# Kernel tuning notes

Hardware: AMD Instinct MI355X
Metric: run time of the kernel (lower is better)

The kernel has to match this reference:

```python
import jax, jax.numpy as jnp
import numpy as np
from jax import lax

EPS = 1e-5
DW_THRESH = 4.0
PW_THRESH = 1e-3


def setup_inputs() -> dict:
    key = jax.random.key(0)
    ks = jax.random.split(key, 13)
    B, C, O, H, W = 32, 256, 256, 56, 56
    inp = {
        "x": jax.random.normal(ks[0], (B, C, H, W), jnp.float32),
        "dw_w": jax.random.normal(ks[1], (C, 1, 3, 3), jnp.float32) * 0.2,
        "dw_b": jax.random.normal(ks[2], (C,), jnp.float32) * 0.1,
        "bn1_gamma": 0.5 + jax.random.uniform(ks[3], (C,), jnp.float32) * 1.5,
        "bn1_beta": jax.random.normal(ks[4], (C,), jnp.float32) * 0.5,
        "bn1_mean": jax.random.normal(ks[5], (C,), jnp.float32) * 0.1,
        "bn1_var": 0.5 + jax.random.uniform(ks[6], (C,), jnp.float32),
        "pw_w": jax.random.normal(ks[7], (O, C, 1, 1), jnp.float32) * 0.06,
        "pw_b": jax.random.normal(ks[8], (O,), jnp.float32) * 0.1,
        "bn2_gamma": 0.5 + jax.random.uniform(ks[9], (O,), jnp.float32) * 1.5,
        "bn2_beta": jax.random.normal(ks[10], (O,), jnp.float32) * 0.5,
        "bn2_mean": jax.random.normal(ks[11], (O,), jnp.float32) * 0.1,
        "bn2_var": 0.5 + jax.random.uniform(ks[12], (O,), jnp.float32),
    }
    return inp


def _bn(x, gamma, beta, mean, var):
    # inference-mode BatchNorm2d over channel axis 1
    inv = gamma * lax.rsqrt(var + EPS)
    return x * inv[None, :, None, None] + (beta - mean * inv)[None, :, None, None]


def _cut(x, thresh):
    # per-(batch, channel) max-abs pruning: max(max(x), -min(x)) == max(|x|)
    max_abs = jnp.max(jnp.abs(x), axis=(2, 3))  # [B, C]
    return jnp.where((max_abs < thresh)[:, :, None, None], 0.0, x)


def reference(x, dw_w, dw_b, bn1_gamma, bn1_beta, bn1_mean, bn1_var,
              pw_w, pw_b, bn2_gamma, bn2_beta, bn2_mean, bn2_var):
    C = x.shape[1]
    # depthwise 3x3 conv, padding=1, groups=C
    y = lax.conv_general_dilated(
        x, dw_w, window_strides=(1, 1), padding=[(1, 1), (1, 1)],
        feature_group_count=C,
        dimension_numbers=("NCHW", "OIHW", "NCHW"),
    ) + dw_b[None, :, None, None]
    y = jax.nn.relu(_bn(y, bn1_gamma, bn1_beta, bn1_mean, bn1_var))
    y = _cut(y, DW_THRESH)
    # pointwise 1x1 conv as channel contraction
    z = jnp.einsum("bihw,oi->bohw", y, pw_w[:, :, 0, 0]) + pw_b[None, :, None, None]
    z = jax.nn.relu(_bn(z, bn2_gamma, bn2_beta, bn2_mean, bn2_var))
    z = _cut(z, PW_THRESH)
    return z
```

## Files before the change

### kernel.cpp

```cpp
#include <hip/hip_runtime.h>
#include <hip/hip_bf16.h>
#include <stdint.h>

#define BATCH 32
#define CIN   256
#define COUT  256
#define HW    3136
#define NPAD  3200

#define AS1 __attribute__((address_space(1)))
#define AS3 __attribute__((address_space(3)))

typedef short bf16x8 __attribute__((ext_vector_type(8)));
typedef float f32x4  __attribute__((ext_vector_type(4)));

__device__ __forceinline__ unsigned short f2bf(float f) {
    unsigned u = __float_as_uint(f);
    u += 0x7fffu + ((u >> 16) & 1u);
    return (unsigned short)(u >> 16);
}

__global__ __launch_bounds__(256) void prep_kernel(
        const float* __restrict__ pw_w, const float* __restrict__ pw_b,
        const float* __restrict__ g2, const float* __restrict__ be2,
        const float* __restrict__ mu2, const float* __restrict__ va2,
        unsigned short* __restrict__ Wp, float* __restrict__ b2,
        unsigned* __restrict__ pwmax) {
    int o = blockIdx.x;
    int t = threadIdx.x;
    float inv2 = g2[o] * rsqrtf(va2[o] + 1e-5f);
    Wp[o * CIN + t] = f2bf(pw_w[o * CIN + t] * inv2);
    if (t == 0) b2[o] = pw_b[o] * inv2 + be2[o] - mu2[o] * inv2;
    int idx = blockIdx.x * 256 + t;
    if (idx < BATCH * COUT) pwmax[idx] = 0u;
}

__global__ __launch_bounds__(256) void dw_kernel(
        const float* __restrict__ x, const float* __restrict__ dww,
        const float* __restrict__ dwb,
        const float* __restrict__ g1, const float* __restrict__ be1,
        const float* __restrict__ mu1, const float* __restrict__ va1,
        unsigned short* __restrict__ y) {
    __shared__ float xs[4 * 3136];
    int tid  = threadIdx.x;
    int lane = tid & 63, wid = tid >> 6;
    int plane = blockIdx.x * 4 + wid;
    int c = plane & 255;

    const float* xp = x + (size_t)plane * HW;
    float* xw = xs + wid * 3136;

#pragma unroll
    for (int i = 0; i < 12; ++i)
        __builtin_amdgcn_global_load_lds(
            (const AS1 void*)(xp + i * 256 + lane * 4),
            (AS3 void*)(xw + i * 256), 16, 0, 0);
    __builtin_amdgcn_global_load_lds(
        (const AS1 void*)(xp + 3072 + lane),
        (AS3 void*)(xw + 3072), 4, 0, 0);

    float w00 = dww[c*9+0], w01 = dww[c*9+1], w02 = dww[c*9+2];
    float w10 = dww[c*9+3], w11 = dww[c*9+4], w12 = dww[c*9+5];
    float w20 = dww[c*9+6], w21 = dww[c*9+7], w22 = dww[c*9+8];
    float inv = g1[c] * rsqrtf(va1[c] + 1e-5f);
    float b0  = dwb[c] * inv + (be1[c] - mu1[c] * inv);

    int  col    = lane < 56 ? lane : 55;
    bool active = lane < 56;
    if (lane == 0)  { w00 = 0.f; w10 = 0.f; w20 = 0.f; }
    if (lane >= 55) { w02 = 0.f; w12 = 0.f; w22 = 0.f; }
    int il = (lane == 0) ? 0 : col - 1;
    int ir = (col == 55) ? 55 : col + 1;

    asm volatile("s_waitcnt vmcnt(0)" ::: "memory");
    __builtin_amdgcn_sched_barrier(0);

    const float* xb = xw;
    unsigned short* yp = y + (size_t)plane * NPAD + col;

    float A = 0.f;
    float Bv = 0.f;
    float lmax = 0.f;
#pragma unroll
    for (int q = 0; q < 56; q += 2) {
        float l0 = xb[q*56 + il],      c0 = xb[q*56 + col],      r0 = xb[q*56 + ir];
        float l1 = xb[(q+1)*56 + il],  c1 = xb[(q+1)*56 + col],  r1 = xb[(q+1)*56 + ir];
        if (q > 0) {
            float o0 = fmaf(l0, w20, fmaf(c0, w21, fmaf(r0, w22, A)));
            float v = fmaxf(fmaf(o0, inv, b0), 0.f);
            if (active) { lmax = fmaxf(lmax, v); yp[(q-1)*56] = f2bf(v); }
        }
        {
            float o1 = fmaf(l0, w10, fmaf(c0, w11, fmaf(r0, w12,
                       fmaf(l1, w20, fmaf(c1, w21, fmaf(r1, w22, Bv))))));
            float v = fmaxf(fmaf(o1, inv, b0), 0.f);
            if (active) { lmax = fmaxf(lmax, v); yp[q*56] = f2bf(v); }
        }
        float top0 = fmaf(l0, w00, fmaf(c0, w01, r0 * w02));
        A  = fmaf(l1, w10, fmaf(c1, w11, fmaf(r1, w12, top0)));
        Bv = fmaf(l1, w00, fmaf(c1, w01, r1 * w02));
    }
    {
        float v = fmaxf(fmaf(A, inv, b0), 0.f);
        if (active) { lmax = fmaxf(lmax, v); yp[55*56] = f2bf(v); }
    }
    for (int off = 32; off >= 1; off >>= 1)
        lmax = fmaxf(lmax, __shfl_xor(lmax, off, 64));
    if (lane < 8) *(uint4*)(y + (size_t)plane * NPAD + HW + lane * 8)
        = make_uint4(0, 0, 0, 0);
    if (lmax < 4.0f) {
        asm volatile("s_waitcnt vmcnt(0)" ::: "memory");
        unsigned short* yp0 = y + (size_t)plane * NPAD;
#pragma unroll
        for (int it = 0; it < 7; ++it) {
            int idx = it * 64 + lane;
            if (idx < 392) *(uint4*)(yp0 + idx * 8) = make_uint4(0, 0, 0, 0);
        }
    }
}

__global__ __launch_bounds__(256, 3) void pw_kernel(
        const unsigned short* __restrict__ y, const unsigned short* __restrict__ Wp,
        const float* __restrict__ b2, float* __restrict__ z,
        unsigned* __restrict__ pwmax) {
    __shared__ __align__(16) char lds[32768 + 16384];
    char* Al = lds;

    int bid0 = blockIdx.x;
    int bid  = (bid0 & 7) * 400 + (bid0 >> 3);
    int nt   = bid % 25;
    int rest = bid / 25;
    int ot   = rest & 3;
    int b    = rest >> 2;
    int o0 = ot * 64, n0 = nt * 128;

    int tid = threadIdx.x, lane = tid & 63, wid = tid >> 6;
    char* Bw = lds + 32768 + wid * 4096;
    int wn = wid * 32;
    int l15 = lane & 15, l4 = lane >> 4;

    const unsigned short* yb = y + (size_t)b * CIN * NPAD;

#pragma unroll
    for (int i = 0; i < 8; ++i) {
        int s = i * 256 + tid;
        int m = s >> 5, cch = s & 31, dch = cch ^ (m & 7);
        __builtin_amdgcn_global_load_lds(
            (const AS1 void*)(Wp + (size_t)(o0 + m) * CIN + dch * 8),
            (AS3 void*)(Al + i * 4096 + wid * 1024), 16, 0, 0);
    }

    int l3 = lane & 7, q3 = lane >> 3;
    const unsigned short* bbase = yb + n0 + wn + l3 * 4 + (size_t)(q3 * 4) * NPAD;

    uint2 praw[2][4];
#define LOADB(kk) { _Pragma("unroll") for (int i = 0; i < 2; ++i)             \
                    _Pragma("unroll") for (int r = 0; r < 4; ++r)             \
                      praw[i][r] = *(const uint2*)(bbase +                    \
                          ((size_t)(kk) * 64 + i * 32 + r) * NPAD); }

#define PACKB() { _Pragma("unroll") for (int i = 0; i < 2; ++i) {             \
        int q = i * 8 + q3;                                                   \
        uint2 r0 = praw[i][0], r1 = praw[i][1], r2 = praw[i][2], r3 = praw[i][3]; \
        _Pragma("unroll") for (int i2 = 0; i2 < 4; ++i2) {                    \
            unsigned x0 = (i2 & 2) ? r0.y : r0.x;                             \
            unsigned x1 = (i2 & 2) ? r1.y : r1.x;                             \
            unsigned x2 = (i2 & 2) ? r2.y : r2.x;                             \
            unsigned x3 = (i2 & 2) ? r3.y : r3.x;                             \
            if (i2 & 1) { x0 >>= 16; x2 >>= 16; }                             \
            else        { x0 &= 0xffffu; x2 &= 0xffffu; }                     \
            unsigned px = (i2 & 1) ? (x0 | (x1 & 0xffff0000u)) : (x0 | (x1 << 16)); \
            unsigned py = (i2 & 1) ? (x2 | (x3 & 0xffff0000u)) : (x2 | (x3 << 16)); \
            int nloc = l3 * 4 + i2;                                           \
            int sb = nloc * 128 + (((q >> 1) ^ ((nloc >> 2) & 7)) << 4) + ((q & 1) << 3); \
            *(uint2*)(Bw + sb) = make_uint2(px, py);                          \
        } } }

#define LGKM0 { asm volatile("s_waitcnt lgkmcnt(0)" ::: "memory");            \
                __builtin_amdgcn_sched_barrier(0); }

    f32x4 acc[4][2];
#pragma unroll
    for (int mf = 0; mf < 4; ++mf)
#pragma unroll
        for (int nf = 0; nf < 2; ++nf) acc[mf][nf] = {0.f, 0.f, 0.f, 0.f};

#define STEP(kk) { _Pragma("unroll") for (int h = 0; h < 2; ++h) {            \
        bf16x8 afr[4], bfr[2];                                                \
        int cc = (kk) * 8 + h * 4 + l4;                                       \
        _Pragma("unroll") for (int mf = 0; mf < 4; ++mf) {                    \
            int m = mf * 16 + l15;                                            \
            afr[mf] = *(const bf16x8*)(Al + m * 512 + ((cc ^ (m & 7)) << 4)); } \
        int cb = h * 4 + l4;                                                  \
        _Pragma("unroll") for (int nf = 0; nf < 2; ++nf) {                    \
            int nloc = nf * 16 + l15;                                         \
            bfr[nf] = *(const bf16x8*)(Bw + nloc * 128 + ((cb ^ ((nloc >> 2) & 7)) << 4)); } \
        _Pragma("unroll") for (int mf = 0; mf < 4; ++mf)                      \
            _Pragma("unroll") for (int nf = 0; nf < 2; ++nf)                  \
                acc[mf][nf] = __builtin_amdgcn_mfma_f32_16x16x32_bf16(        \
                    afr[mf], bfr[nf], acc[mf][nf], 0, 0, 0); } }

    LOADB(0);
    asm volatile("s_waitcnt vmcnt(8)" ::: "memory");
    __builtin_amdgcn_sched_barrier(0);
    __builtin_amdgcn_s_barrier();
    __builtin_amdgcn_sched_barrier(0);
    PACKB();
    LGKM0;
    LOADB(1);

    STEP(0);
    PACKB(); LGKM0; LOADB(2);
    STEP(1);
    PACKB(); LGKM0; LOADB(3);
    STEP(2);
    PACKB(); LGKM0;
    STEP(3);

#undef LOADB
#undef PACKB
#undef STEP

    float* zb = z + (size_t)b * COUT * HW;
#pragma unroll
    for (int mf = 0; mf < 4; ++mf) {
        int obase = o0 + mf * 16 + l4 * 4;
        float bb0 = b2[obase + 0], bb1 = b2[obase + 1];
        float bb2v = b2[obase + 2], bb3 = b2[obase + 3];
        float rmax[4] = {0.f, 0.f, 0.f, 0.f};
#pragma unroll
        for (int nf = 0; nf < 2; ++nf) {
            int n = n0 + wn + nf * 16 + l15;
            bool valid = (n < HW);
            float v0 = fmaxf(acc[mf][nf][0] + bb0, 0.f);
            float v1 = fmaxf(acc[mf][nf][1] + bb1, 0.f);
            float v2 = fmaxf(acc[mf][nf][2] + bb2v, 0.f);
            float v3 = fmaxf(acc[mf][nf][3] + bb3, 0.f);
            if (valid) {
                zb[(size_t)(obase + 0) * HW + n] = v0;
                zb[(size_t)(obase + 1) * HW + n] = v1;
                zb[(size_t)(obase + 2) * HW + n] = v2;
                zb[(size_t)(obase + 3) * HW + n] = v3;
                rmax[0] = fmaxf(rmax[0], v0);
                rmax[1] = fmaxf(rmax[1], v1);
                rmax[2] = fmaxf(rmax[2], v2);
                rmax[3] = fmaxf(rmax[3], v3);
            }
        }
#pragma unroll
        for (int r = 0; r < 4; ++r) {
            float v = rmax[r];
            v = fmaxf(v, __shfl_xor(v, 1, 64));
            v = fmaxf(v, __shfl_xor(v, 2, 64));
            v = fmaxf(v, __shfl_xor(v, 4, 64));
            v = fmaxf(v, __shfl_xor(v, 8, 64));
            if (l15 == 0)
                atomicMax(&pwmax[b * COUT + obase + r], __float_as_uint(v));
        }
    }
}

__global__ __launch_bounds__(256) void cut_kernel(const unsigned* __restrict__ pwmax,
                                                  float* __restrict__ z) {
    int base = blockIdx.x * 8;
#pragma unroll
    for (int j = 0; j < 8; ++j) {
        int bo = base + j;
        if (__uint_as_float(pwmax[bo]) >= 1e-3f) continue;
        float4* zp = (float4*)(z + (size_t)bo * HW);
        for (int i = threadIdx.x; i < HW / 4; i += 256)
            zp[i] = make_float4(0.f, 0.f, 0.f, 0.f);
    }
}

extern "C" void kernel_launch(void* const* d_in, const int* in_sizes, int n_in,
                              void* d_out, int out_size, void* d_ws, size_t ws_size,
                              hipStream_t stream) {
    const float* x   = (const float*)d_in[0];
    const float* dww = (const float*)d_in[1];
    const float* dwb = (const float*)d_in[2];
    const float* g1  = (const float*)d_in[3];
    const float* be1 = (const float*)d_in[4];
    const float* mu1 = (const float*)d_in[5];
    const float* va1 = (const float*)d_in[6];
    const float* pww = (const float*)d_in[7];
    const float* pwb = (const float*)d_in[8];
    const float* g2  = (const float*)d_in[9];
    const float* be2 = (const float*)d_in[10];
    const float* mu2 = (const float*)d_in[11];
    const float* va2 = (const float*)d_in[12];
    float* z = (float*)d_out;

    char* ws = (char*)d_ws;
    const size_t Y_BYTES = (size_t)BATCH * CIN * NPAD * 2;
    unsigned short* y  = (unsigned short*)ws;
    unsigned short* Wp = (unsigned short*)(ws + Y_BYTES);
    float* b2          = (float*)(ws + Y_BYTES + 131072);
    unsigned* pwmax    = (unsigned*)(ws + Y_BYTES + 131072 + 1024);

    prep_kernel<<<256, 256, 0, stream>>>(pww, pwb, g2, be2, mu2, va2, Wp, b2, pwmax);
    dw_kernel<<<2048, 256, 0, stream>>>(x, dww, dwb, g1, be1, mu1, va1, y);
    pw_kernel<<<3200, 256, 0, stream>>>(y, Wp, b2, z, pwmax);
    cut_kernel<<<BATCH * COUT / 8, 256, 0, stream>>>(pwmax, z);
}
```

Before: 121.5 us.

## Process two batches per pw block to reuse loaded weight tile, double-buffer B

The pointwise GEMM kernel now handles two batch images per block, so the 64x256 weight tile loaded into LDS once is reused across both batches, and the grid halves. The B operand is staged through two shared LDS buffers, with loads for the next k-step issued before packing the current one, and the waves are rearranged into a 2x2 tile over M and N instead of splitting only over N. This cuts redundant weight loads and per-block setup, at the cost of 64KB LDS, lower occupancy (2 blocks per CU) and a barrier per k-step.

Result: faster. 100.4 us (-17.3%).

```diff
diff --git a/kernel.cpp b/kernel.cpp
--- a/kernel.cpp
+++ b/kernel.cpp
@@ -119,27 +119,48 @@
     }
 }
 
-__global__ __launch_bounds__(256, 3) void pw_kernel(
+__device__ __forceinline__ void pack_b(const uint2* src, char* dstbase,
+                                       const int* sb_) {
+    uint2 r0 = src[0], r1 = src[1], r2 = src[2], r3 = src[3];
+#pragma unroll
+    for (int i2 = 0; i2 < 4; ++i2) {
+        unsigned x0 = (i2 & 2) ? r0.y : r0.x;
+        unsigned x1 = (i2 & 2) ? r1.y : r1.x;
+        unsigned x2 = (i2 & 2) ? r2.y : r2.x;
+        unsigned x3 = (i2 & 2) ? r3.y : r3.x;
+        if (i2 & 1) { x0 >>= 16; x2 >>= 16; }
+        else        { x0 &= 0xffffu; x2 &= 0xffffu; }
+        unsigned px = (i2 & 1) ? (x0 | (x1 & 0xffff0000u)) : (x0 | (x1 << 16));
+        unsigned py = (i2 & 1) ? (x2 | (x3 & 0xffff0000u)) : (x2 | (x3 << 16));
+        *(uint2*)(dstbase + sb_[i2]) = make_uint2(px, py);
+    }
+}
+
+__global__ __launch_bounds__(256, 2) void pw_kernel(
         const unsigned short* __restrict__ y, const unsigned short* __restrict__ Wp,
         const float* __restrict__ b2, float* __restrict__ z,
         unsigned* __restrict__ pwmax) {
-    __shared__ __align__(16) char lds[32768 + 16384];
-    char* Al = lds;
+    __shared__ __align__(16) char lds[65536];
+    char* Al  = lds;
+    char* Bl0 = lds + 32768;
+    char* Bl1 = lds + 49152;
 
     int bid0 = blockIdx.x;
-    int bid  = (bid0 & 7) * 400 + (bid0 >> 3);
-    int nt   = bid % 25;
-    int rest = bid / 25;
-    int ot   = rest & 3;
-    int b    = rest >> 2;
+    int bid  = (bid0 & 7) * 200 + (bid0 >> 3);
+    int ot   = bid & 3;
+    int rest = bid >> 2;
+    int nt   = rest % 25;
+    int bg   = rest / 25;
     int o0 = ot * 64, n0 = nt * 128;
-
-    int tid = threadIdx.x, lane = tid & 63, wid = tid >> 6;
-    char* Bw = lds + 32768 + wid * 4096;
-    int wn = wid * 32;
+    int b0 = bg * 2, b1 = b0 + 1;
+
+    int tid = threadIdx.x;
+    int lane = tid & 63, wid = tid >> 6;
+    int wm = (wid >> 1) * 32, wn = (wid & 1) * 64;
     int l15 = lane & 15, l4 = lane >> 4;
 
-    const unsigned short* yb = y + (size_t)b * CIN * NPAD;
+    const unsigned short* yb0 = y + (size_t)b0 * CIN * NPAD;
+    const unsigned short* yb1 = y + (size_t)b1 * CIN * NPAD;
 
 #pragma unroll
     for (int i = 0; i < 8; ++i) {
@@ -150,114 +171,109 @@
             (AS3 void*)(Al + i * 4096 + wid * 1024), 16, 0, 0);
     }
 
-    int l3 = lane & 7, q3 = lane >> 3;
-    const unsigned short* bbase = yb + n0 + wn + l3 * 4 + (size_t)(q3 * 4) * NPAD;
-
-    uint2 praw[2][4];
-#define LOADB(kk) { _Pragma("unroll") for (int i = 0; i < 2; ++i)             \
-                    _Pragma("unroll") for (int r = 0; r < 4; ++r)             \
-                      praw[i][r] = *(const uint2*)(bbase +                    \
-                          ((size_t)(kk) * 64 + i * 32 + r) * NPAD); }
-
-#define PACKB() { _Pragma("unroll") for (int i = 0; i < 2; ++i) {             \
-        int q = i * 8 + q3;                                                   \
-        uint2 r0 = praw[i][0], r1 = praw[i][1], r2 = praw[i][2], r3 = praw[i][3]; \
-        _Pragma("unroll") for (int i2 = 0; i2 < 4; ++i2) {                    \
-            unsigned x0 = (i2 & 2) ? r0.y : r0.x;                             \
-            unsigned x1 = (i2 & 2) ? r1.y : r1.x;                             \
-            unsigned x2 = (i2 & 2) ? r2.y : r2.x;                             \
-            unsigned x3 = (i2 & 2) ? r3.y : r3.x;                             \
-            if (i2 & 1) { x0 >>= 16; x2 >>= 16; }                             \
-            else        { x0 &= 0xffffu; x2 &= 0xffffu; }                     \
-            unsigned px = (i2 & 1) ? (x0 | (x1 & 0xffff0000u)) : (x0 | (x1 << 16)); \
-            unsigned py = (i2 & 1) ? (x2 | (x3 & 0xffff0000u)) : (x2 | (x3 << 16)); \
-            int nloc = l3 * 4 + i2;                                           \
-            int sb = nloc * 128 + (((q >> 1) ^ ((nloc >> 2) & 7)) << 4) + ((q & 1) << 3); \
-            *(uint2*)(Bw + sb) = make_uint2(px, py);                          \
-        } } }
-
-#define LGKM0 { asm volatile("s_waitcnt lgkmcnt(0)" ::: "memory");            \
+    int q = tid >> 5, nq = tid & 31;
+    size_t boff = (size_t)(q * 8) * NPAD + n0 + nq * 4;
+    int sbA[4], sbB[4];
+#pragma unroll
+    for (int i2 = 0; i2 < 4; ++i2) {
+        int nloc = nq * 4 + i2;
+        sbA[i2] = nloc * 128 + ((q ^ ((nloc >> 2) & 7)) << 4);
+        sbB[i2] = sbA[i2] + 8;
+    }
+
+    uint2 praw0[8], praw1[8];
+#define LOADB(dst, ybp, kk) { _Pragma("unroll")                              \
+    for (int r = 0; r < 8; ++r)                                              \
+        dst[r] = *(const uint2*)((ybp) + boff + (size_t)((kk) * 64 + r) * NPAD); }
+#define PACKB(src, Blb) { pack_b(src, Blb, sbA); pack_b(src + 4, Blb, sbB); }
+#define VM8   { asm volatile("s_waitcnt vmcnt(8)" ::: "memory"); __builtin_amdgcn_sched_barrier(0); }
+#define VM0   { asm volatile("s_waitcnt vmcnt(0)" ::: "memory"); __builtin_amdgcn_sched_barrier(0); }
+#define LGBAR { asm volatile("s_waitcnt lgkmcnt(0)" ::: "memory");           \
+                __builtin_amdgcn_sched_barrier(0);                           \
+                __builtin_amdgcn_s_barrier();                                \
                 __builtin_amdgcn_sched_barrier(0); }
 
-    f32x4 acc[4][2];
-#pragma unroll
-    for (int mf = 0; mf < 4; ++mf)
-#pragma unroll
-        for (int nf = 0; nf < 2; ++nf) acc[mf][nf] = {0.f, 0.f, 0.f, 0.f};
-
-#define STEP(kk) { _Pragma("unroll") for (int h = 0; h < 2; ++h) {            \
-        bf16x8 afr[4], bfr[2];                                                \
-        int cc = (kk) * 8 + h * 4 + l4;                                       \
-        _Pragma("unroll") for (int mf = 0; mf < 4; ++mf) {                    \
-            int m = mf * 16 + l15;                                            \
+    f32x4 accA[2][4], accB[2][4];
+#pragma unroll
+    for (int mf = 0; mf < 2; ++mf)
+#pragma unroll
+        for (int nf = 0; nf < 4; ++nf) {
+            accA[mf][nf] = {0.f, 0.f, 0.f, 0.f};
+            accB[mf][nf] = {0.f, 0.f, 0.f, 0.f};
+        }
+
+#define STEPM(ACC, KK, BLB) { _Pragma("unroll") for (int h = 0; h < 2; ++h) { \
+        bf16x8 afr[2], bfr[4];                                                \
+        int cc = (KK) * 8 + h * 4 + l4;                                       \
+        _Pragma("unroll") for (int mf = 0; mf < 2; ++mf) {                    \
+            int m = wm + mf * 16 + l15;                                       \
             afr[mf] = *(const bf16x8*)(Al + m * 512 + ((cc ^ (m & 7)) << 4)); } \
         int cb = h * 4 + l4;                                                  \
-        _Pragma("unroll") for (int nf = 0; nf < 2; ++nf) {                    \
-            int nloc = nf * 16 + l15;                                         \
-            bfr[nf] = *(const bf16x8*)(Bw + nloc * 128 + ((cb ^ ((nloc >> 2) & 7)) << 4)); } \
-        _Pragma("unroll") for (int mf = 0; mf < 4; ++mf)                      \
-            _Pragma("unroll") for (int nf = 0; nf < 2; ++nf)                  \
-                acc[mf][nf] = __builtin_amdgcn_mfma_f32_16x16x32_bf16(        \
-                    afr[mf], bfr[nf], acc[mf][nf], 0, 0, 0); } }
-
-    LOADB(0);
-    asm volatile("s_waitcnt vmcnt(8)" ::: "memory");
-    __builtin_amdgcn_sched_barrier(0);
+        _Pragma("unroll") for (int nf = 0; nf < 4; ++nf) {                    \
+            int n = wn + nf * 16 + l15;                                       \
+            bfr[nf] = *(const bf16x8*)((BLB) + n * 128 + ((cb ^ ((n >> 2) & 7)) << 4)); } \
+        _Pragma("unroll") for (int mf = 0; mf < 2; ++mf)                      \
+            _Pragma("unroll") for (int nf = 0; nf < 4; ++nf)                  \
+                ACC[mf][nf] = __builtin_amdgcn_mfma_f32_16x16x32_bf16(        \
+                    afr[mf], bfr[nf], ACC[mf][nf], 0, 0, 0); } }
+
+    LOADB(praw0, yb0, 0);
+    VM8;
     __builtin_amdgcn_s_barrier();
     __builtin_amdgcn_sched_barrier(0);
-    PACKB();
-    LGKM0;
-    LOADB(1);
-
-    STEP(0);
-    PACKB(); LGKM0; LOADB(2);
-    STEP(1);
-    PACKB(); LGKM0; LOADB(3);
-    STEP(2);
-    PACKB(); LGKM0;
-    STEP(3);
+
+    LOADB(praw1, yb0, 1); VM8; PACKB(praw0, Bl0); LGBAR; STEPM(accA, 0, Bl0);
+    LOADB(praw0, yb0, 2); VM8; PACKB(praw1, Bl1); LGBAR; STEPM(accA, 1, Bl1);
+    LOADB(praw1, yb0, 3); VM8; PACKB(praw0, Bl0); LGBAR; STEPM(accA, 2, Bl0);
+    LOADB(praw0, yb1, 0); VM8; PACKB(praw1, Bl1); LGBAR; STEPM(accA, 3, Bl1);
+    LOADB(praw1, yb1, 1); VM8; PACKB(praw0, Bl0); LGBAR; STEPM(accB, 0, Bl0);
+    LOADB(praw0, yb1, 2); VM8; PACKB(praw1, Bl1); LGBAR; STEPM(accB, 1, Bl1);
+    LOADB(praw1, yb1, 3); VM8; PACKB(praw0, Bl0); LGBAR; STEPM(accB, 2, Bl0);
+    VM0;                       PACKB(praw1, Bl1); LGBAR; STEPM(accB, 3, Bl1);
 
 #undef LOADB
 #undef PACKB
-#undef STEP
-
-    float* zb = z + (size_t)b * COUT * HW;
-#pragma unroll
-    for (int mf = 0; mf < 4; ++mf) {
-        int obase = o0 + mf * 16 + l4 * 4;
-        float bb0 = b2[obase + 0], bb1 = b2[obase + 1];
-        float bb2v = b2[obase + 2], bb3 = b2[obase + 3];
-        float rmax[4] = {0.f, 0.f, 0.f, 0.f};
-#pragma unroll
-        for (int nf = 0; nf < 2; ++nf) {
-            int n = n0 + wn + nf * 16 + l15;
-            bool valid = (n < HW);
-            float v0 = fmaxf(acc[mf][nf][0] + bb0, 0.f);
-            float v1 = fmaxf(acc[mf][nf][1] + bb1, 0.f);
-            float v2 = fmaxf(acc[mf][nf][2] + bb2v, 0.f);
-            float v3 = fmaxf(acc[mf][nf][3] + bb3, 0.f);
-            if (valid) {
-                zb[(size_t)(obase + 0) * HW + n] = v0;
-                zb[(size_t)(obase + 1) * HW + n] = v1;
-                zb[(size_t)(obase + 2) * HW + n] = v2;
-                zb[(size_t)(obase + 3) * HW + n] = v3;
-                rmax[0] = fmaxf(rmax[0], v0);
-                rmax[1] = fmaxf(rmax[1], v1);
-                rmax[2] = fmaxf(rmax[2], v2);
-                rmax[3] = fmaxf(rmax[3], v3);
-            }
-        }
-#pragma unroll
-        for (int r = 0; r < 4; ++r) {
-            float v = rmax[r];
-            v = fmaxf(v, __shfl_xor(v, 1, 64));
-            v = fmaxf(v, __shfl_xor(v, 2, 64));
-            v = fmaxf(v, __shfl_xor(v, 4, 64));
-            v = fmaxf(v, __shfl_xor(v, 8, 64));
-            if (l15 == 0)
-                atomicMax(&pwmax[b * COUT + obase + r], __float_as_uint(v));
-        }
-    }
+#undef STEPM
+
+#define EPI(BI, ACC) {                                                        \
+    float* zb = z + (size_t)(BI) * COUT * HW;                                 \
+    _Pragma("unroll") for (int mf = 0; mf < 2; ++mf) {                        \
+        int obase = o0 + wm + mf * 16 + l4 * 4;                               \
+        float bb0 = b2[obase + 0], bb1 = b2[obase + 1];                       \
+        float bb2v = b2[obase + 2], bb3 = b2[obase + 3];                      \
+        float rmax[4] = {0.f, 0.f, 0.f, 0.f};                                 \
+        _Pragma("unroll") for (int nf = 0; nf < 4; ++nf) {                    \
+            int n = n0 + wn + nf * 16 + l15;                                  \
+            bool valid = (n < HW);                                            \
+            float v0 = fmaxf(ACC[mf][nf][0] + bb0, 0.f);                      \
+            float v1 = fmaxf(ACC[mf][nf][1] + bb1, 0.f);                      \
+            float v2 = fmaxf(ACC[mf][nf][2] + bb2v, 0.f);                     \
+            float v3 = fmaxf(ACC[mf][nf][3] + bb3, 0.f);                      \
+            if (valid) {                                                      \
+                zb[(size_t)(obase + 0) * HW + n] = v0;                        \
+                zb[(size_t)(obase + 1) * HW + n] = v1;                        \
+                zb[(size_t)(obase + 2) * HW + n] = v2;                        \
+                zb[(size_t)(obase + 3) * HW + n] = v3;                        \
+                rmax[0] = fmaxf(rmax[0], v0);                                 \
+                rmax[1] = fmaxf(rmax[1], v1);                                 \
+                rmax[2] = fmaxf(rmax[2], v2);                                 \
+                rmax[3] = fmaxf(rmax[3], v3);                                 \
+            }                                                                 \
+        }                                                                     \
+        _Pragma("unroll") for (int r = 0; r < 4; ++r) {                       \
+            float v = rmax[r];                                                \
+            v = fmaxf(v, __shfl_xor(v, 1, 64));                               \
+            v = fmaxf(v, __shfl_xor(v, 2, 64));                               \
+            v = fmaxf(v, __shfl_xor(v, 4, 64));                               \
+            v = fmaxf(v, __shfl_xor(v, 8, 64));                               \
+            if (l15 == 0)                                                     \
+                atomicMax(&pwmax[(BI) * COUT + obase + r], __float_as_uint(v)); \
+        }                                                                     \
+    } }
+
+    EPI(b0, accA);
+    EPI(b1, accB);
+#undef EPI
 }
 
 __global__ __launch_bounds__(256) void cut_kernel(const unsigned* __restrict__ pwmax,
@@ -300,6 +316,6 @@
 
     prep_kernel<<<256, 256, 0, stream>>>(pww, pwb, g2, be2, mu2, va2, Wp, b2, pwmax);
     dw_kernel<<<2048, 256, 0, stream>>>(x, dww, dwb, g1, be1, mu1, va1, y);
-    pw_kernel<<<3200, 256, 0, stream>>>(y, Wp, b2, z, pwmax);
+    pw_kernel<<<1600, 256, 0, stream>>>(y, Wp, b2, z, pwmax);
     cut_kernel<<<BATCH * COUT / 8, 256, 0, stream>>>(pwmax, z);
 }
```

## Retile pointwise GEMM to full-O per block with register-staged A and double-buffered B

Applied to the files above, without the earlier changes.

The pointwise kernel now gives each block all 256 output channels for a 64-column spatial tile, one 64-channel slice per wave. Weight fragments load straight from global into registers and B tiles are double-buffered in per-wave LDS, with a software pipeline over eight K steps. The 3136-wide spatial dimension now splits into 49 exact tiles, so padding columns and bounds checks go away. Per-plane maxima are written as partial values that the cut kernel reduces, replacing atomics and the zero-init in prep. The cost is more register pressure from the 4x4 accumulators and each wave reading its own weight slice from global memory rather than sharing it through LDS.

Result: faster. 100.9 us (-16.9%).

```diff
diff --git a/kernel.cpp b/kernel.cpp
--- a/kernel.cpp
+++ b/kernel.cpp
@@ -24,15 +24,12 @@
         const float* __restrict__ pw_w, const float* __restrict__ pw_b,
         const float* __restrict__ g2, const float* __restrict__ be2,
         const float* __restrict__ mu2, const float* __restrict__ va2,
-        unsigned short* __restrict__ Wp, float* __restrict__ b2,
-        unsigned* __restrict__ pwmax) {
+        unsigned short* __restrict__ Wp, float* __restrict__ b2) {
     int o = blockIdx.x;
     int t = threadIdx.x;
     float inv2 = g2[o] * rsqrtf(va2[o] + 1e-5f);
     Wp[o * CIN + t] = f2bf(pw_w[o * CIN + t] * inv2);
     if (t == 0) b2[o] = pw_b[o] * inv2 + be2[o] - mu2[o] * inv2;
-    int idx = blockIdx.x * 256 + t;
-    if (idx < BATCH * COUT) pwmax[idx] = 0u;
 }
 
 __global__ __launch_bounds__(256) void dw_kernel(
@@ -122,104 +119,115 @@
 __global__ __launch_bounds__(256, 3) void pw_kernel(
         const unsigned short* __restrict__ y, const unsigned short* __restrict__ Wp,
         const float* __restrict__ b2, float* __restrict__ z,
-        unsigned* __restrict__ pwmax) {
-    __shared__ __align__(16) char lds[32768 + 16384];
-    char* Al = lds;
+        float* __restrict__ pwpart) {
+    __shared__ __align__(16) char lds[32768];
+    int tid = threadIdx.x;
+    int lane = tid & 63, wid = tid >> 6;
+    char* B0 = lds + wid * 8192;
+    char* B1 = B0 + 4096;
 
     int bid0 = blockIdx.x;
-    int bid  = (bid0 & 7) * 400 + (bid0 >> 3);
-    int nt   = bid % 25;
-    int rest = bid / 25;
-    int ot   = rest & 3;
-    int b    = rest >> 2;
-    int o0 = ot * 64, n0 = nt * 128;
-
-    int tid = threadIdx.x, lane = tid & 63, wid = tid >> 6;
-    char* Bw = lds + 32768 + wid * 4096;
-    int wn = wid * 32;
+    int bid  = (bid0 & 7) * 196 + (bid0 >> 3);
+    int b  = bid / 49;
+    int nt = bid - b * 49;
+    int n0 = nt * 64;
+    int o0 = wid * 64;
+
     int l15 = lane & 15, l4 = lane >> 4;
 
-    const unsigned short* yb = y + (size_t)b * CIN * NPAD;
-
-#pragma unroll
-    for (int i = 0; i < 8; ++i) {
-        int s = i * 256 + tid;
-        int m = s >> 5, cch = s & 31, dch = cch ^ (m & 7);
-        __builtin_amdgcn_global_load_lds(
-            (const AS1 void*)(Wp + (size_t)(o0 + m) * CIN + dch * 8),
-            (AS3 void*)(Al + i * 4096 + wid * 1024), 16, 0, 0);
-    }
-
-    int l3 = lane & 7, q3 = lane >> 3;
-    const unsigned short* bbase = yb + n0 + wn + l3 * 4 + (size_t)(q3 * 4) * NPAD;
-
-    uint2 praw[2][4];
-#define LOADB(kk) { _Pragma("unroll") for (int i = 0; i < 2; ++i)             \
-                    _Pragma("unroll") for (int r = 0; r < 4; ++r)             \
-                      praw[i][r] = *(const uint2*)(bbase +                    \
-                          ((size_t)(kk) * 64 + i * 32 + r) * NPAD); }
-
-#define PACKB() { _Pragma("unroll") for (int i = 0; i < 2; ++i) {             \
-        int q = i * 8 + q3;                                                   \
-        uint2 r0 = praw[i][0], r1 = praw[i][1], r2 = praw[i][2], r3 = praw[i][3]; \
-        _Pragma("unroll") for (int i2 = 0; i2 < 4; ++i2) {                    \
-            unsigned x0 = (i2 & 2) ? r0.y : r0.x;                             \
-            unsigned x1 = (i2 & 2) ? r1.y : r1.x;                             \
-            unsigned x2 = (i2 & 2) ? r2.y : r2.x;                             \
-            unsigned x3 = (i2 & 2) ? r3.y : r3.x;                             \
-            if (i2 & 1) { x0 >>= 16; x2 >>= 16; }                             \
-            else        { x0 &= 0xffffu; x2 &= 0xffffu; }                     \
-            unsigned px = (i2 & 1) ? (x0 | (x1 & 0xffff0000u)) : (x0 | (x1 << 16)); \
-            unsigned py = (i2 & 1) ? (x2 | (x3 & 0xffff0000u)) : (x2 | (x3 << 16)); \
-            int nloc = l3 * 4 + i2;                                           \
-            int sb = nloc * 128 + (((q >> 1) ^ ((nloc >> 2) & 7)) << 4) + ((q & 1) << 3); \
-            *(uint2*)(Bw + sb) = make_uint2(px, py);                          \
-        } } }
-
-#define LGKM0 { asm volatile("s_waitcnt lgkmcnt(0)" ::: "memory");            \
-                __builtin_amdgcn_sched_barrier(0); }
-
-    f32x4 acc[4][2];
+    int k4 = lane >> 4, nq = lane & 15;
+    const unsigned short* bsrc = y + (size_t)b * CIN * NPAD
+                               + (size_t)(k4 * 8) * NPAD + n0 + nq * 4;
+    int sbA[4], sbB[4];
+#pragma unroll
+    for (int i2 = 0; i2 < 4; ++i2) {
+        int nloc = nq * 4 + i2;
+        sbA[i2] = nloc * 64 + ((k4 ^ ((nloc >> 2) & 3)) << 4);
+        sbB[i2] = sbA[i2] + 8;
+    }
+    const unsigned short* asrcA = Wp + (size_t)(o0 + l15) * CIN + l4 * 8;
+
+    uint2 pr0[8], pr1[8];
+    bf16x8 afA[4], afB[4];
+
+#define LOADB(dst, s) { _Pragma("unroll") for (int r = 0; r < 8; ++r)        \
+    dst[r] = *(const uint2*)(bsrc + (size_t)((s) * 32 + r) * NPAD); }
+#define LOADA(dst, s) { _Pragma("unroll") for (int mf = 0; mf < 4; ++mf)     \
+    dst[mf] = *(const bf16x8*)(asrcA + mf * 16 * CIN + (s) * 32); }
+#define PIN  __builtin_amdgcn_sched_barrier(0);
+#define VM12 { asm volatile("s_waitcnt vmcnt(12)" ::: "memory"); PIN }
+#define VM0  { asm volatile("s_waitcnt vmcnt(0)"  ::: "memory"); PIN }
+#define LG   { asm volatile("s_waitcnt lgkmcnt(0)" ::: "memory"); PIN }
+
+#define PACK4(src, q, dst, sb_) {                                            \
+    uint2 r0 = src[0], r1 = src[1], r2 = src[2], r3 = src[3];                \
+    _Pragma("unroll") for (int i2 = 0; i2 < 4; ++i2) {                       \
+        unsigned x0 = (i2 & 2) ? r0.y : r0.x;                                \
+        unsigned x1 = (i2 & 2) ? r1.y : r1.x;                                \
+        unsigned x2 = (i2 & 2) ? r2.y : r2.x;                                \
+        unsigned x3 = (i2 & 2) ? r3.y : r3.x;                                \
+        if (i2 & 1) { x0 >>= 16; x2 >>= 16; }                                \
+        else        { x0 &= 0xffffu; x2 &= 0xffffu; }                        \
+        unsigned px = (i2 & 1) ? (x0 | (x1 & 0xffff0000u)) : (x0 | (x1 << 16)); \
+        unsigned py = (i2 & 1) ? (x2 | (x3 & 0xffff0000u)) : (x2 | (x3 << 16)); \
+        *(uint2*)((dst) + (sb_)[i2]) = make_uint2(px, py);                   \
+    } }
+#define PACK8(pr, dst) { PACK4(pr, 0, dst, sbA); PACK4((pr + 4), 1, dst, sbB); }
+
+    f32x4 acc[4][4];
 #pragma unroll
     for (int mf = 0; mf < 4; ++mf)
 #pragma unroll
-        for (int nf = 0; nf < 2; ++nf) acc[mf][nf] = {0.f, 0.f, 0.f, 0.f};
-
-#define STEP(kk) { _Pragma("unroll") for (int h = 0; h < 2; ++h) {            \
-        bf16x8 afr[4], bfr[2];                                                \
-        int cc = (kk) * 8 + h * 4 + l4;                                       \
-        _Pragma("unroll") for (int mf = 0; mf < 4; ++mf) {                    \
-            int m = mf * 16 + l15;                                            \
-            afr[mf] = *(const bf16x8*)(Al + m * 512 + ((cc ^ (m & 7)) << 4)); } \
-        int cb = h * 4 + l4;                                                  \
-        _Pragma("unroll") for (int nf = 0; nf < 2; ++nf) {                    \
-            int nloc = nf * 16 + l15;                                         \
-            bfr[nf] = *(const bf16x8*)(Bw + nloc * 128 + ((cb ^ ((nloc >> 2) & 7)) << 4)); } \
-        _Pragma("unroll") for (int mf = 0; mf < 4; ++mf)                      \
-            _Pragma("unroll") for (int nf = 0; nf < 2; ++nf)                  \
-                acc[mf][nf] = __builtin_amdgcn_mfma_f32_16x16x32_bf16(        \
-                    afr[mf], bfr[nf], acc[mf][nf], 0, 0, 0); } }
-
-    LOADB(0);
-    asm volatile("s_waitcnt vmcnt(8)" ::: "memory");
-    __builtin_amdgcn_sched_barrier(0);
-    __builtin_amdgcn_s_barrier();
-    __builtin_amdgcn_sched_barrier(0);
-    PACKB();
-    LGKM0;
-    LOADB(1);
-
-    STEP(0);
-    PACKB(); LGKM0; LOADB(2);
-    STEP(1);
-    PACKB(); LGKM0; LOADB(3);
-    STEP(2);
-    PACKB(); LGKM0;
-    STEP(3);
+        for (int nf = 0; nf < 4; ++nf) acc[mf][nf] = {0.f, 0.f, 0.f, 0.f};
+
+#define STEPC(AF, BUF) {                                                     \
+    bf16x8 bfr[4];                                                           \
+    _Pragma("unroll") for (int nf = 0; nf < 4; ++nf) {                       \
+        int n = nf * 16 + l15;                                               \
+        bfr[nf] = *(const bf16x8*)((BUF) + n * 64 + ((l4 ^ ((n >> 2) & 3)) << 4)); } \
+    _Pragma("unroll") for (int mf = 0; mf < 4; ++mf)                         \
+        _Pragma("unroll") for (int nf = 0; nf < 4; ++nf)                     \
+            acc[mf][nf] = __builtin_amdgcn_mfma_f32_16x16x32_bf16(           \
+                AF[mf], bfr[nf], acc[mf][nf], 0, 0, 0); }
+
+    LOADA(afA, 0); LOADB(pr0, 0); PIN;
+    LOADA(afB, 1); LOADB(pr1, 1); PIN;
+    VM12; PACK8(pr0, B0); LG;
+
+    STEPC(afA, B0);
+    LOADA(afA, 2); LOADB(pr0, 2); PIN;
+    VM12; PACK8(pr1, B1); LG;
+
+    STEPC(afB, B1);
+    LOADA(afB, 3); LOADB(pr1, 3); PIN;
+    VM12; PACK8(pr0, B0); LG;
+
+    STEPC(afA, B0);
+    LOADA(afA, 4); LOADB(pr0, 4); PIN;
+    VM12; PACK8(pr1, B1); LG;
+
+    STEPC(afB, B1);
+    LOADA(afB, 5); LOADB(pr1, 5); PIN;
+    VM12; PACK8(pr0, B0); LG;
+
+    STEPC(afA, B0);
+    LOADA(afA, 6); LOADB(pr0, 6); PIN;
+    VM12; PACK8(pr1, B1); LG;
+
+    STEPC(afB, B1);
+    LOADA(afB, 7); LOADB(pr1, 7); PIN;
+    VM12; PACK8(pr0, B0); LG;
+
+    STEPC(afA, B0);
+    VM0; PACK8(pr1, B1); LG;
+
+    STEPC(afB, B1);
 
 #undef LOADB
-#undef PACKB
-#undef STEP
+#undef LOADA
+#undef PACK4
+#undef PACK8
+#undef STEPC
 
     float* zb = z + (size_t)b * COUT * HW;
 #pragma unroll
@@ -229,23 +237,20 @@
         float bb2v = b2[obase + 2], bb3 = b2[obase + 3];
         float rmax[4] = {0.f, 0.f, 0.f, 0.f};
 #pragma unroll
-        for (int nf = 0; nf < 2; ++nf) {
-            int n = n0 + wn + nf * 16 + l15;
-            bool valid = (n < HW);
+        for (int nf = 0; nf < 4; ++nf) {
+            int n = n0 + nf * 16 + l15;
             float v0 = fmaxf(acc[mf][nf][0] + bb0, 0.f);
             float v1 = fmaxf(acc[mf][nf][1] + bb1, 0.f);
             float v2 = fmaxf(acc[mf][nf][2] + bb2v, 0.f);
             float v3 = fmaxf(acc[mf][nf][3] + bb3, 0.f);
-            if (valid) {
-                zb[(size_t)(obase + 0) * HW + n] = v0;
-                zb[(size_t)(obase + 1) * HW + n] = v1;
-                zb[(size_t)(obase + 2) * HW + n] = v2;
-                zb[(size_t)(obase + 3) * HW + n] = v3;
-                rmax[0] = fmaxf(rmax[0], v0);
-                rmax[1] = fmaxf(rmax[1], v1);
-                rmax[2] = fmaxf(rmax[2], v2);
-                rmax[3] = fmaxf(rmax[3], v3);
-            }
+            zb[(size_t)(obase + 0) * HW + n] = v0;
+            zb[(size_t)(obase + 1) * HW + n] = v1;
+            zb[(size_t)(obase + 2) * HW + n] = v2;
+            zb[(size_t)(obase + 3) * HW + n] = v3;
+            rmax[0] = fmaxf(rmax[0], v0);
+            rmax[1] = fmaxf(rmax[1], v1);
+            rmax[2] = fmaxf(rmax[2], v2);
+            rmax[3] = fmaxf(rmax[3], v3);
         }
 #pragma unroll
         for (int r = 0; r < 4; ++r) {
@@ -255,22 +260,24 @@
             v = fmaxf(v, __shfl_xor(v, 4, 64));
             v = fmaxf(v, __shfl_xor(v, 8, 64));
             if (l15 == 0)
-                atomicMax(&pwmax[b * COUT + obase + r], __float_as_uint(v));
-        }
-    }
-}
-
-__global__ __launch_bounds__(256) void cut_kernel(const unsigned* __restrict__ pwmax,
+                pwpart[(size_t)(b * COUT + obase + r) * 49 + nt] = v;
+        }
+    }
+}
+
+__global__ __launch_bounds__(256) void cut_kernel(const float* __restrict__ pwpart,
                                                   float* __restrict__ z) {
-    int base = blockIdx.x * 8;
-#pragma unroll
-    for (int j = 0; j < 8; ++j) {
-        int bo = base + j;
-        if (__uint_as_float(pwmax[bo]) >= 1e-3f) continue;
-        float4* zp = (float4*)(z + (size_t)bo * HW);
-        for (int i = threadIdx.x; i < HW / 4; i += 256)
-            zp[i] = make_float4(0.f, 0.f, 0.f, 0.f);
-    }
+    int plane = blockIdx.x * 8 + (threadIdx.x >> 5);
+    int l = threadIdx.x & 31;
+    float m = 0.f;
+    for (int i = l; i < 49; i += 32)
+        m = fmaxf(m, pwpart[(size_t)plane * 49 + i]);
+    for (int off = 16; off >= 1; off >>= 1)
+        m = fmaxf(m, __shfl_xor(m, off, 32));
+    if (m >= 1e-3f) return;
+    float4* zp = (float4*)(z + (size_t)plane * HW);
+    for (int i = l; i < HW / 4; i += 32)
+        zp[i] = make_float4(0.f, 0.f, 0.f, 0.f);
 }
 
 extern "C" void kernel_launch(void* const* d_in, const int* in_sizes, int n_in,
@@ -296,10 +303,10 @@
     unsigned short* y  = (unsigned short*)ws;
     unsigned short* Wp = (unsigned short*)(ws + Y_BYTES);
     float* b2          = (float*)(ws + Y_BYTES + 131072);
-    unsigned* pwmax    = (unsigned*)(ws + Y_BYTES + 131072 + 1024);
-
-    prep_kernel<<<256, 256, 0, stream>>>(pww, pwb, g2, be2, mu2, va2, Wp, b2, pwmax);
+    float* pwpart      = (float*)(ws + Y_BYTES + 131072 + 1024);
+
+    prep_kernel<<<256, 256, 0, stream>>>(pww, pwb, g2, be2, mu2, va2, Wp, b2);
     dw_kernel<<<2048, 256, 0, stream>>>(x, dww, dwb, g1, be1, mu1, va1, y);
-    pw_kernel<<<3200, 256, 0, stream>>>(y, Wp, b2, z, pwmax);
-    cut_kernel<<<BATCH * COUT / 8, 256, 0, stream>>>(pwmax, z);
-}
+    pw_kernel<<<BATCH * 49, 256, 0, stream>>>(y, Wp, b2, z, pwpart);
+    cut_kernel<<<BATCH * COUT / 8, 256, 0, stream>>>(pwpart, z);
+}
```
